# Kernel tuning notes

Measured on AMD Instinct MI355X. Metric: run time of the kernel, lower is better.

## Reference

```python
import jax, jax.numpy as jnp
import numpy as np

TAU = 0.5

def setup_inputs() -> dict:
    key = jax.random.key(0)
    ks = jax.random.split(key, 9)
    B, N, C, T, R = 32, 196, 768, 10, 16
    s = 0.02
    return {
        "x": jax.random.normal(ks[0], (B, N, C), jnp.float32),
        "W_qkv": jax.random.normal(ks[1], (3 * C, C), jnp.float32) * s,
        "b_qkv": jax.random.normal(ks[2], (3 * C,), jnp.float32) * s,
        "A_q": jax.random.normal(ks[3], (T, R, C), jnp.float32) * s,
        "B_q": jax.random.normal(ks[4], (T, C, R), jnp.float32) * s,
        "A_v": jax.random.normal(ks[5], (T, R, C), jnp.float32) * s,
        "B_v": jax.random.normal(ks[6], (T, C, R), jnp.float32) * s,
        "gate_logits_q": jax.random.normal(ks[7], (T,), jnp.float32),
        "gate_logits_v": jax.random.normal(ks[8], (T,), jnp.float32),
    }

def _fro(w):
    # Frobenius norm per task: w is [T, d1, d2]
    return jnp.sqrt(jnp.sum(w * w, axis=(1, 2)))

def _lora_branch(x, A, B, logits):
    # x: [B,N,C]; A: [T,R,C]; B: [T,C,R]; logits: [T]
    gate = jax.nn.softmax(logits / TAU)                      # soft gumbel gate, eval (no noise)
    scale = gate / (_fro(A) * _fro(B))                       # fuse 1/(||A||*||B||) with gate weight
    tmp = jnp.einsum('bnc,trc->tbnr', x, A)                  # low-rank projections, all tasks batched
    return jnp.einsum('tbnr,tcr,t->bnc', tmp, B, scale)      # up-project + weighted sum over tasks

def reference(x, W_qkv, b_qkv, A_q, B_q, A_v, B_v, gate_logits_q, gate_logits_v):
    C = x.shape[-1]
    qkv = jnp.einsum('bnc,dc->bnd', x, W_qkv) + b_qkv        # [B,N,3C]
    new_q = _lora_branch(x, A_q, B_q, gate_logits_q)
    new_v = _lora_branch(x, A_v, B_v, gate_logits_v)
    qkv = qkv.at[:, :, :C].add(new_q)
    qkv = qkv.at[:, :, 2 * C:].add(new_v)
    return qkv
```

## Files before the change

### kernel.cpp

```cpp
#include <hip/hip_runtime.h>

#define TAU_INV 2.0f

typedef unsigned short u16;
typedef short bf16x8 __attribute__((ext_vector_type(8)));
typedef float f32x4 __attribute__((ext_vector_type(4)));
typedef u16 u16x4v __attribute__((ext_vector_type(4)));
typedef u16 u16x8v __attribute__((ext_vector_type(8)));

typedef __attribute__((address_space(1))) const void GASV;
typedef __attribute__((address_space(3))) void LASV;
#define GLOAD16(gp, lp) __builtin_amdgcn_global_load_lds((GASV*)(gp), (LASV*)(lp), 16, 0, 0)

__device__ __forceinline__ u16 f2bf(float f) {
  unsigned u = __float_as_uint(f);
  u += 0x7FFFu + ((u >> 16) & 1u);
  return (u16)(u >> 16);
}

__global__ __launch_bounds__(256) void k_prep(
    const float* __restrict__ x, u16* __restrict__ xb,
    const float* __restrict__ Aq, const float* __restrict__ Bq,
    const float* __restrict__ Av, const float* __restrict__ Bv,
    const float* __restrict__ lq, const float* __restrict__ lv,
    float* __restrict__ scales) {
  const int bid = blockIdx.x;
  const int tid = threadIdx.x;
  if (bid < 2352) {
    const int i = (bid * 256 + tid) * 8;
    float4 v0 = *(const float4*)(x + i);
    float4 v1 = *(const float4*)(x + i + 4);
    u16x8v o;
    o[0] = f2bf(v0.x); o[1] = f2bf(v0.y); o[2] = f2bf(v0.z); o[3] = f2bf(v0.w);
    o[4] = f2bf(v1.x); o[5] = f2bf(v1.y); o[6] = f2bf(v1.z); o[7] = f2bf(v1.w);
    *(u16x8v*)(xb + i) = o;
    return;
  }
  const int sb = bid - 2352;
  const int br = sb / 10, t = sb % 10;
  const float* __restrict__ A = br ? Av : Aq;
  const float* __restrict__ B = br ? Bv : Bq;
  const float* __restrict__ lg = br ? lv : lq;
  const float4* A4 = (const float4*)(A + t * 12288);
  const float4* B4 = (const float4*)(B + t * 12288);
  float sA = 0.f, sB = 0.f;
  for (int i = tid; i < 3072; i += 256) {
    float4 a = A4[i];
    float4 b = B4[i];
    sA += a.x * a.x + a.y * a.y + a.z * a.z + a.w * a.w;
    sB += b.x * b.x + b.y * b.y + b.z * b.z + b.w * b.w;
  }
  for (int off = 32; off; off >>= 1) {
    sA += __shfl_down(sA, off);
    sB += __shfl_down(sB, off);
  }
  __shared__ float rA[4], rB[4];
  if ((tid & 63) == 0) { rA[tid >> 6] = sA; rB[tid >> 6] = sB; }
  __syncthreads();
  if (tid == 0) {
    sA = rA[0] + rA[1] + rA[2] + rA[3];
    sB = rB[0] + rB[1] + rB[2] + rB[3];
    float mx = -1e30f;
    for (int j = 0; j < 10; ++j) mx = fmaxf(mx, lg[j] * TAU_INV);
    float den = 0.f, num = 0.f;
    for (int j = 0; j < 10; ++j) {
      float e = __expf(lg[j] * TAU_INV - mx);
      den += e;
      if (j == t) num = e;
    }
    scales[br * 16 + t] = (num / den) * rsqrtf(sA) * rsqrtf(sB);
  }
}

__global__ __launch_bounds__(256) void k_dwpack(
    const float* __restrict__ Aq, const float* __restrict__ Bq,
    const float* __restrict__ Av, const float* __restrict__ Bv,
    const float* __restrict__ W, const float* __restrict__ scales,
    u16* __restrict__ Weff) {
  const int bid = blockIdx.x;
  const int tid = threadIdx.x;
  if (bid >= 72) {
    const int base = 589824 + (bid - 72) * 16384;
#pragma unroll
    for (int it = 0; it < 8; ++it) {
      const int i = base + (it * 256 + tid) * 8;
      float4 v0 = *(const float4*)(W + i);
      float4 v1 = *(const float4*)(W + i + 4);
      u16x8v o;
      o[0] = f2bf(v0.x); o[1] = f2bf(v0.y); o[2] = f2bf(v0.z); o[3] = f2bf(v0.w);
      o[4] = f2bf(v1.x); o[5] = f2bf(v1.y); o[6] = f2bf(v1.z); o[7] = f2bf(v1.w);
      *(u16x8v*)(Weff + i) = o;
    }
    return;
  }
  const int br = bid / 36, t36 = bid % 36;
  const int tm = t36 / 6, tn = t36 % 6;
  const float* __restrict__ A = br ? Av : Aq;
  const float* __restrict__ B = br ? Bv : Bq;
  const int d0 = tm * 128, c0 = tn * 128;
  const int rowbase = br ? 1536 : 0;
  __shared__ u16 As[128 * 32];
  __shared__ u16 Bs[128 * 32];
  const int lane = tid & 63, w = tid >> 6, wm = w >> 1, wn = w & 1;
  const int lr = lane & 15, kb = lane >> 4;
  f32x4 acc[4][4];
#pragma unroll
  for (int i = 0; i < 4; ++i)
#pragma unroll
    for (int j = 0; j < 4; ++j)
#pragma unroll
      for (int e = 0; e < 4; ++e) acc[i][j][e] = 0.f;

  for (int it = 0; it < 5; ++it) {
    const int k0 = it * 32;
    if (it) __syncthreads();
#pragma unroll
    for (int i = 0; i < 4; ++i) {
      int q = tid + i * 256;
      int d = q >> 3;
      int k = (q & 7) * 4;
      int kg = k0 + k;
      int t = kg >> 4, r = kg & 15;
      float4 v = *(const float4*)(B + (t * 768 + d0 + d) * 16 + r);
      float s = scales[br * 16 + t];
      u16x4v o;
      o[0] = f2bf(v.x * s); o[1] = f2bf(v.y * s);
      o[2] = f2bf(v.z * s); o[3] = f2bf(v.w * s);
      *(u16x4v*)(As + q * 4) = o;
    }
#pragma unroll
    for (int i = 0; i < 4; ++i) {
      int q = tid + i * 256;
      int c = (q & 31) * 4;
      int kk = q >> 5;
      float4 v = *(const float4*)(A + (k0 + kk) * 768 + c0 + c);
      Bs[(c + 0) * 32 + kk] = f2bf(v.x);
      Bs[(c + 1) * 32 + kk] = f2bf(v.y);
      Bs[(c + 2) * 32 + kk] = f2bf(v.z);
      Bs[(c + 3) * 32 + kk] = f2bf(v.w);
    }
    __syncthreads();
    bf16x8 a[4], b[4];
#pragma unroll
    for (int i = 0; i < 4; ++i)
      a[i] = *(const bf16x8*)(As + (wm * 64 + i * 16 + lr) * 32 + kb * 8);
#pragma unroll
    for (int j = 0; j < 4; ++j)
      b[j] = *(const bf16x8*)(Bs + (wn * 64 + j * 16 + lr) * 32 + kb * 8);
#pragma unroll
    for (int i = 0; i < 4; ++i)
#pragma unroll
      for (int j = 0; j < 4; ++j)
        acc[i][j] = __builtin_amdgcn_mfma_f32_16x16x32_bf16(a[i], b[j], acc[i][j], 0, 0, 0);
  }
#pragma unroll
  for (int i = 0; i < 4; ++i)
#pragma unroll
    for (int jn = 0; jn < 4; ++jn)
#pragma unroll
      for (int j = 0; j < 4; ++j) {
        int row = rowbase + d0 + wm * 64 + i * 16 + kb * 4 + j;
        int col = c0 + wn * 64 + jn * 16 + lr;
        int g = row * 768 + col;
        Weff[g] = f2bf(W[g] + acc[i][jn][j]);
      }
}

__global__ __launch_bounds__(256, 4) void k_gemm(
    const u16* __restrict__ Xb,
    const u16* __restrict__ Wb,
    const float* __restrict__ bias,
    float* __restrict__ out) {
  const int b = blockIdx.x;
  const int xcd = b & 7, sub = b >> 3;
  const int wgid = (xcd < 2 ? xcd * 111 : 222 + (xcd - 2) * 110) + sub;
  const int tn = wgid % 18, tm = wgid / 18;
  const int m0 = tm * 128, n0 = tn * 128;
  __shared__ u16 As[2][128 * 32];
  __shared__ u16 Bs[2][128 * 32];
  const int tid = threadIdx.x;
  const int lane = tid & 63, w = tid >> 6, wm = w >> 1, wn = w & 1;
  const int lr = lane & 15, kb = lane >> 4;
  f32x4 acc[4][4];
#pragma unroll
  for (int i = 0; i < 4; ++i)
#pragma unroll
    for (int j = 0; j < 4; ++j)
#pragma unroll
      for (int e = 0; e < 4; ++e) acc[i][j][e] = 0.f;

  const int r0 = tid >> 2;
  const int cb0 = (tid & 3) * 8;
  const u16* gA0 = Xb + (m0 + r0) * 768 + cb0;
  const u16* gA1 = gA0 + 64 * 768;
  const u16* gB0 = Wb + (n0 + r0) * 768 + cb0;
  const u16* gB1 = gB0 + 64 * 768;
  const int wbase = (tid & 192) * 16;

#define STAGE(buf, kt)                                            \
  {                                                               \
    const int ko_ = (kt) * 32;                                    \
    char* lA_ = (char*)&As[(buf)][0] + wbase;                     \
    char* lB_ = (char*)&Bs[(buf)][0] + wbase;                     \
    GLOAD16(gA0 + ko_, lA_);                                      \
    GLOAD16(gA1 + ko_, lA_ + 4096);                               \
    GLOAD16(gB0 + ko_, lB_);                                      \
    GLOAD16(gB1 + ko_, lB_ + 4096);                               \
  }

  STAGE(0, 0)
  STAGE(1, 1)

  for (int kt = 0; kt < 24; ++kt) {
    const int cur = kt & 1;
    if (kt < 23) {
      asm volatile("s_waitcnt vmcnt(4)" ::: "memory");
    } else {
      asm volatile("s_waitcnt vmcnt(0)" ::: "memory");
    }
    __builtin_amdgcn_s_barrier();
    asm volatile("" ::: "memory");
    {
      const u16* Ab = &As[cur][0];
      const u16* Bb = &Bs[cur][0];
      bf16x8 a[4], bfr[4];
#pragma unroll
      for (int i = 0; i < 4; ++i)
        a[i] = *(const bf16x8*)(Ab + (wm * 64 + i * 16 + lr) * 32 + kb * 8);
#pragma unroll
      for (int j = 0; j < 4; ++j)
        bfr[j] = *(const bf16x8*)(Bb + (wn * 64 + j * 16 + lr) * 32 + kb * 8);
#pragma unroll
      for (int i = 0; i < 4; ++i)
#pragma unroll
        for (int j = 0; j < 4; ++j)
          acc[i][j] = __builtin_amdgcn_mfma_f32_16x16x32_bf16(a[i], bfr[j], acc[i][j], 0, 0, 0);
    }
    asm volatile("" ::: "memory");
    __builtin_amdgcn_s_barrier();
    asm volatile("" ::: "memory");
    if (kt < 22) STAGE(cur, kt + 2)
  }
#undef STAGE

  float br4[4];
#pragma unroll
  for (int jn = 0; jn < 4; ++jn) br4[jn] = bias[n0 + wn * 64 + jn * 16 + lr];
#pragma unroll
  for (int i = 0; i < 4; ++i)
#pragma unroll
    for (int jn = 0; jn < 4; ++jn)
#pragma unroll
      for (int j = 0; j < 4; ++j) {
        int m = m0 + wm * 64 + i * 16 + kb * 4 + j;
        int n = n0 + wn * 64 + jn * 16 + lr;
        out[m * 2304 + n] = acc[i][jn][j] + br4[jn];
      }
}

extern "C" void kernel_launch(void* const* d_in, const int* in_sizes, int n_in,
                              void* d_out, int out_size, void* d_ws, size_t ws_size,
                              hipStream_t stream) {
  const float* x    = (const float*)d_in[0];
  const float* Wq   = (const float*)d_in[1];
  const float* bqkv = (const float*)d_in[2];
  const float* Aq   = (const float*)d_in[3];
  const float* Bq   = (const float*)d_in[4];
  const float* Av   = (const float*)d_in[5];
  const float* Bv   = (const float*)d_in[6];
  const float* lq   = (const float*)d_in[7];
  const float* lv   = (const float*)d_in[8];
  float* out = (float*)d_out;

  char* ws = (char*)d_ws;
  float* scales = (float*)ws;
  u16* xb   = (u16*)(ws + 256);
  u16* weff = (u16*)(ws + 256 + 9633792);

  k_prep<<<2372, 256, 0, stream>>>(x, xb, Aq, Bq, Av, Bv, lq, lv, scales);
  k_dwpack<<<108, 256, 0, stream>>>(Aq, Bq, Av, Bv, Wq, scales, weff);
  k_gemm<<<882, 256, 0, stream>>>(xb, weff, bqkv, out);
}
```

Baseline: 168.4 us.

## Rewrite GEMM with 256x256 tiles, swizzled LDS and interleaved load/MFMA phases

Replaces the 128x128, BK=32 GEMM with a 512-thread 256x256 tile kernel using BK=64 double buffering and XOR-swizzled LDS addressing. Global-to-LDS staging is split into quarter-chunks placed between MFMA phases, and the MFMA blocks run at raised wave priority. The aim is more data reuse per load, fewer LDS bank conflicts and better overlap of loads with math. In exchange, only 225 workgroups are launched, occupancy per CU drops, the X buffer is padded to 6400 rows, and output stores are masked.

```diff
diff --git a/kernel.cpp b/kernel.cpp
--- a/kernel.cpp
+++ b/kernel.cpp
@@ -166,96 +166,143 @@
       }
 }
 
-__global__ __launch_bounds__(256, 4) void k_gemm(
+__global__ __launch_bounds__(512, 2) void k_gemm(
     const u16* __restrict__ Xb,
     const u16* __restrict__ Wb,
     const float* __restrict__ bias,
     float* __restrict__ out) {
   const int b = blockIdx.x;
   const int xcd = b & 7, sub = b >> 3;
-  const int wgid = (xcd < 2 ? xcd * 111 : 222 + (xcd - 2) * 110) + sub;
-  const int tn = wgid % 18, tm = wgid / 18;
-  const int m0 = tm * 128, n0 = tn * 128;
-  __shared__ u16 As[2][128 * 32];
-  __shared__ u16 Bs[2][128 * 32];
+  const int wgid = (xcd == 0) ? sub : (29 + (xcd - 1) * 28 + sub);
+  const int tn = wgid % 9, tm = wgid / 9;
+  const int m0 = tm * 256, n0 = tn * 256;
+  __shared__ char lds[131072];
   const int tid = threadIdx.x;
-  const int lane = tid & 63, w = tid >> 6, wm = w >> 1, wn = w & 1;
+  const int lane = tid & 63;
+  const int w = tid >> 6, wm = w >> 2, wn = w & 3;
   const int lr = lane & 15, kb = lane >> 4;
-  f32x4 acc[4][4];
-#pragma unroll
-  for (int i = 0; i < 4; ++i)
+  const int cs0 = ((kb ^ (lr & 7)) << 4);
+  const int cs1 = (((4 + kb) ^ (lr & 7)) << 4);
+  const int arow = (wm * 128 + lr) << 7;
+  const int brow = (wn * 64 + lr) << 7;
+  const int r0 = tid >> 3;
+  const int cb0 = (((tid & 7) ^ (r0 & 7)) << 3);
+  const u16* pA = Xb + (m0 + r0) * 768 + cb0;
+  const u16* pB = Wb + (n0 + r0) * 768 + cb0;
+  const int wb = (tid >> 6) << 10;
+
+  f32x4 acc[8][4];
+#pragma unroll
+  for (int i = 0; i < 8; ++i)
 #pragma unroll
     for (int j = 0; j < 4; ++j)
 #pragma unroll
       for (int e = 0; e < 4; ++e) acc[i][j][e] = 0.f;
 
-  const int r0 = tid >> 2;
-  const int cb0 = (tid & 3) * 8;
-  const u16* gA0 = Xb + (m0 + r0) * 768 + cb0;
-  const u16* gA1 = gA0 + 64 * 768;
-  const u16* gB0 = Wb + (n0 + r0) * 768 + cb0;
-  const u16* gB1 = gB0 + 64 * 768;
-  const int wbase = (tid & 192) * 16;
-
-#define STAGE(buf, kt)                                            \
-  {                                                               \
-    const int ko_ = (kt) * 32;                                    \
-    char* lA_ = (char*)&As[(buf)][0] + wbase;                     \
-    char* lB_ = (char*)&Bs[(buf)][0] + wbase;                     \
-    GLOAD16(gA0 + ko_, lA_);                                      \
-    GLOAD16(gA1 + ko_, lA_ + 4096);                               \
-    GLOAD16(gB0 + ko_, lB_);                                      \
-    GLOAD16(gB1 + ko_, lB_ + 4096);                               \
-  }
-
-  STAGE(0, 0)
-  STAGE(1, 1)
-
-  for (int kt = 0; kt < 24; ++kt) {
+#define STG_A(buf, kt, h)                                                        \
+  {                                                                              \
+    GLOAD16(pA + ((h)*128 + 0) * 768 + (kt)*64, lds + (buf)*32768 + (h)*16384 + 0 + wb);    \
+    GLOAD16(pA + ((h)*128 + 64) * 768 + (kt)*64, lds + (buf)*32768 + (h)*16384 + 8192 + wb);\
+  }
+#define STG_B(buf, kt, h)                                                        \
+  {                                                                              \
+    GLOAD16(pB + ((h)*128 + 0) * 768 + (kt)*64, lds + 65536 + (buf)*32768 + (h)*16384 + 0 + wb);    \
+    GLOAD16(pB + ((h)*128 + 64) * 768 + (kt)*64, lds + 65536 + (buf)*32768 + (h)*16384 + 8192 + wb);\
+  }
+#define LDA8(buf, mh)                                                            \
+  {                                                                              \
+    const char* p_ = lds + (buf)*32768 + arow + (mh)*8192;                       \
+    a[0] = *(const bf16x8*)(p_ + 0 * 2048 + cs0);                                \
+    a[1] = *(const bf16x8*)(p_ + 0 * 2048 + cs1);                                \
+    a[2] = *(const bf16x8*)(p_ + 1 * 2048 + cs0);                                \
+    a[3] = *(const bf16x8*)(p_ + 1 * 2048 + cs1);                                \
+    a[4] = *(const bf16x8*)(p_ + 2 * 2048 + cs0);                                \
+    a[5] = *(const bf16x8*)(p_ + 2 * 2048 + cs1);                                \
+    a[6] = *(const bf16x8*)(p_ + 3 * 2048 + cs0);                                \
+    a[7] = *(const bf16x8*)(p_ + 3 * 2048 + cs1);                                \
+  }
+#define LDB4(dst, buf, nh)                                                       \
+  {                                                                              \
+    const char* p_ = lds + 65536 + (buf)*32768 + brow + (nh)*4096;               \
+    dst[0] = *(const bf16x8*)(p_ + 0 * 2048 + cs0);                              \
+    dst[1] = *(const bf16x8*)(p_ + 0 * 2048 + cs1);                              \
+    dst[2] = *(const bf16x8*)(p_ + 1 * 2048 + cs0);                              \
+    dst[3] = *(const bf16x8*)(p_ + 1 * 2048 + cs1);                              \
+  }
+#define BAR()                          \
+  {                                    \
+    asm volatile("" ::: "memory");     \
+    __builtin_amdgcn_s_barrier();      \
+    asm volatile("" ::: "memory");     \
+  }
+#define MMQ(QM, QN, BREG)                                                        \
+  {                                                                              \
+    __builtin_amdgcn_s_setprio(1);                                               \
+    _Pragma("unroll") for (int mf = 0; mf < 4; ++mf)                             \
+        _Pragma("unroll") for (int nf = 0; nf < 2; ++nf)                         \
+            _Pragma("unroll") for (int ks = 0; ks < 2; ++ks)                     \
+                acc[(QM)*4 + mf][(QN)*2 + nf] =                                  \
+        __builtin_amdgcn_mfma_f32_16x16x32_bf16(                                 \
+            a[mf * 2 + ks], BREG[nf * 2 + ks], acc[(QM)*4 + mf][(QN)*2 + nf],    \
+            0, 0, 0);                                                            \
+    __builtin_amdgcn_s_setprio(0);                                               \
+  }
+
+  bf16x8 a[8], b0[4], b1[4];
+  STG_A(0, 0, 0) STG_B(0, 0, 0) STG_A(0, 0, 1) STG_B(0, 0, 1)
+  STG_A(1, 1, 0) STG_B(1, 1, 0) STG_A(1, 1, 1) STG_B(1, 1, 1)
+
+#pragma unroll 1
+  for (int kt = 0; kt < 12; ++kt) {
     const int cur = kt & 1;
-    if (kt < 23) {
-      asm volatile("s_waitcnt vmcnt(4)" ::: "memory");
+    if (kt < 11) {
+      asm volatile("s_waitcnt vmcnt(8)" ::: "memory");
     } else {
       asm volatile("s_waitcnt vmcnt(0)" ::: "memory");
     }
-    __builtin_amdgcn_s_barrier();
-    asm volatile("" ::: "memory");
-    {
-      const u16* Ab = &As[cur][0];
-      const u16* Bb = &Bs[cur][0];
-      bf16x8 a[4], bfr[4];
-#pragma unroll
-      for (int i = 0; i < 4; ++i)
-        a[i] = *(const bf16x8*)(Ab + (wm * 64 + i * 16 + lr) * 32 + kb * 8);
-#pragma unroll
-      for (int j = 0; j < 4; ++j)
-        bfr[j] = *(const bf16x8*)(Bb + (wn * 64 + j * 16 + lr) * 32 + kb * 8);
-#pragma unroll
-      for (int i = 0; i < 4; ++i)
-#pragma unroll
-        for (int j = 0; j < 4; ++j)
-          acc[i][j] = __builtin_amdgcn_mfma_f32_16x16x32_bf16(a[i], bfr[j], acc[i][j], 0, 0, 0);
-    }
-    asm volatile("" ::: "memory");
-    __builtin_amdgcn_s_barrier();
-    asm volatile("" ::: "memory");
-    if (kt < 22) STAGE(cur, kt + 2)
-  }
-#undef STAGE
-
-  float br4[4];
-#pragma unroll
-  for (int jn = 0; jn < 4; ++jn) br4[jn] = bias[n0 + wn * 64 + jn * 16 + lr];
-#pragma unroll
-  for (int i = 0; i < 4; ++i)
-#pragma unroll
-    for (int jn = 0; jn < 4; ++jn)
-#pragma unroll
-      for (int j = 0; j < 4; ++j) {
-        int m = m0 + wm * 64 + i * 16 + kb * 4 + j;
-        int n = n0 + wn * 64 + jn * 16 + lr;
-        out[m * 2304 + n] = acc[i][jn][j] + br4[jn];
-      }
+    BAR();
+    LDA8(cur, 0)
+    LDB4(b0, cur, 0)
+    BAR();
+    MMQ(0, 0, b0)
+    BAR();
+    LDB4(b1, cur, 1)
+    BAR();
+    MMQ(0, 1, b1)
+    BAR();
+    LDA8(cur, 1)
+    if (kt < 10) { STG_A(cur, kt + 2, 0) STG_B(cur, kt + 2, 0) }
+    BAR();
+    MMQ(1, 1, b1)
+    BAR();
+    if (kt < 10) { STG_B(cur, kt + 2, 1) }
+    BAR();
+    MMQ(1, 0, b0)
+    BAR();
+    if (kt < 10) { STG_A(cur, kt + 2, 1) }
+  }
+#undef STG_A
+#undef STG_B
+#undef LDA8
+#undef LDB4
+#undef MMQ
+
+  float br[4];
+#pragma unroll
+  for (int q = 0; q < 4; ++q)
+    br[q] = bias[n0 + wn * 64 + (q >> 1) * 32 + (q & 1) * 16 + lr];
+#pragma unroll
+  for (int mh = 0; mh < 2; ++mh)
+#pragma unroll
+    for (int mf = 0; mf < 4; ++mf)
+#pragma unroll
+      for (int q = 0; q < 4; ++q)
+#pragma unroll
+        for (int e = 0; e < 4; ++e) {
+          int m = m0 + wm * 128 + mh * 64 + mf * 16 + kb * 4 + e;
+          int n = n0 + wn * 64 + (q >> 1) * 32 + (q & 1) * 16 + lr;
+          if (m < 6272) out[m * 2304 + n] = acc[mh * 4 + mf][q][e] + br[q];
+        }
 }
 
 extern "C" void kernel_launch(void* const* d_in, const int* in_sizes, int n_in,
@@ -275,9 +322,9 @@
   char* ws = (char*)d_ws;
   float* scales = (float*)ws;
   u16* xb   = (u16*)(ws + 256);
-  u16* weff = (u16*)(ws + 256 + 9633792);
+  u16* weff = (u16*)(ws + 256 + 9830400);
 
   k_prep<<<2372, 256, 0, stream>>>(x, xb, Aq, Bq, Av, Bv, lq, lv, scales);
   k_dwpack<<<108, 256, 0, stream>>>(Aq, Bq, Av, Bv, Wq, scales, weff);
-  k_gemm<<<882, 256, 0, stream>>>(xb, weff, bqkv, out);
-}
+  k_gemm<<<225, 512, 0, stream>>>(xb, weff, bqkv, out);
+}
```

After: 173.6 us. 3.1% more time.
